# Kernel tuning notes

Measured on AMD Instinct MI355X. Metric: run time of the kernel, lower is better.

## Reference

```python
import jax, jax.numpy as jnp
import numpy as np

E = 100000   # n_entities
R = 64       # n_relations
I = 256      # in_channels
O = 256      # out_channels
N_EDGES = 1_600_000


def setup_inputs() -> dict:
    key = jax.random.key(0)
    k1, k2, k3, k4 = jax.random.split(key, 4)
    x = jax.random.normal(k1, (E, I), dtype=jnp.float32)
    # cs must be nonzero (it is reciprocated); uniform in [0.5, 1.5)
    cs = jax.random.uniform(k2, (E, R), dtype=jnp.float32) + 0.5
    W = jax.random.normal(k3, (R, I, O), dtype=jnp.float32) * 0.05
    edge_index = jax.random.randint(k4, (2, N_EDGES), 0, E, dtype=jnp.int64)
    return {"x": x, "cs": cs, "W": W, "edge_index": edge_index}


def reference(x, cs, W, edge_index):
    # Faithful to: torch.einsum('er,rio,ej->eo', 1/cs, W, x)
    # i and j are independently contracted indices, so this factorizes:
    # out[e,o] = (sum_j x[e,j]) * sum_r (1/cs[e,r]) * (sum_i W[r,i,o])
    cs_reciprocal = 1.0 / cs                 # (E, R)
    W_sum = jnp.sum(W, axis=1)               # (R, O)
    x_sum = jnp.sum(x, axis=1)               # (E,)
    src = (cs_reciprocal @ W_sum) * x_sum[:, None]  # (E, O)
    return src
```

## Files before the change

### kernel.cpp

```cpp
#include <hip/hip_runtime.h>


constexpr int En = 100000;
constexpr int Rn = 64;
constexpr int In = 256;
constexpr int On = 256;

__global__ void wsum_kernel(const float* __restrict__ W, float* __restrict__ wsum) {
    const int r = blockIdx.x >> 3;
    const int chunk = blockIdx.x & 7;
    const int o = threadIdx.x;
    const float* base = W + ((size_t)r * In + (size_t)chunk * 32) * On + o;
    float s = 0.f;
#pragma unroll
    for (int i = 0; i < 32; ++i) s += base[(size_t)i * On];
    atomicAdd(&wsum[r * On + o], s);
}

__global__ __launch_bounds__(256) void rgcn_main(const float* __restrict__ x,
                                                 const float* __restrict__ cs,
                                                 const float* __restrict__ wsum,
                                                 float* __restrict__ out) {
    __shared__ float ldsW[Rn * On];
    __shared__ float recipT[Rn * 64];

    const int t = threadIdx.x;
    const int R0 = blockIdx.x * 64;

#pragma unroll
    for (int k = 0; k < 16; ++k) {
        const int f = k * 1024 + t * 4;
        *reinterpret_cast<float4*>(&ldsW[f]) =
            *reinterpret_cast<const float4*>(&wsum[f]);
    }

    const int wv = t >> 6;
    const int lane = t & 63;
#pragma unroll
    for (int s = 0; s < 16; ++s) {
        const int lr = s * 4 + wv;
        const int g = R0 + lr;
        float4 v = make_float4(0.f, 0.f, 0.f, 0.f);
        if (g < En)
            v = *reinterpret_cast<const float4*>(&x[(size_t)g * In + lane * 4]);
        float sum = v.x + v.y + v.z + v.w;
#pragma unroll
        for (int off = 32; off; off >>= 1) sum += __shfl_down(sum, off, 64);
        if (lane == 0) recipT[lr] = sum;
    }
    __syncthreads();

    const int q = t >> 4;
    const int m = t & 15;
    float xs[4];
    float4 c4[4];
#pragma unroll
    for (int s = 0; s < 4; ++s) {
        const int row = s * 16 + q;
        const int g = R0 + row;
        xs[s] = (g < En) ? recipT[row] : 0.f;
        c4[s] = make_float4(1.f, 1.f, 1.f, 1.f);
        if (g < En)
            c4[s] = *reinterpret_cast<const float4*>(&cs[(size_t)g * Rn + m * 4]);
    }
    __syncthreads();

#pragma unroll
    for (int s = 0; s < 4; ++s) {
        const int row = s * 16 + q;
        recipT[(4 * m + 0) * 64 + row] = xs[s] / c4[s].x;
        recipT[(4 * m + 1) * 64 + row] = xs[s] / c4[s].y;
        recipT[(4 * m + 2) * 64 + row] = xs[s] / c4[s].z;
        recipT[(4 * m + 3) * 64 + row] = xs[s] / c4[s].w;
    }
    __syncthreads();

    const int trow = t >> 5;
    const int tcol = t & 31;
    float acc[8][8];
#pragma unroll
    for (int j = 0; j < 8; ++j)
#pragma unroll
        for (int k = 0; k < 8; ++k) acc[j][k] = 0.f;

#pragma unroll 4
    for (int r = 0; r < 64; ++r) {
        const float4 a0 = *reinterpret_cast<float4*>(&recipT[r * 64 + trow * 8]);
        const float4 a1 = *reinterpret_cast<float4*>(&recipT[r * 64 + trow * 8 + 4]);
        const float4 b0 = *reinterpret_cast<float4*>(&ldsW[r * 256 + tcol * 4]);
        const float4 b1 = *reinterpret_cast<float4*>(&ldsW[r * 256 + 128 + tcol * 4]);
        const float a[8] = {a0.x, a0.y, a0.z, a0.w, a1.x, a1.y, a1.z, a1.w};
        const float b[8] = {b0.x, b0.y, b0.z, b0.w, b1.x, b1.y, b1.z, b1.w};
#pragma unroll
        for (int j = 0; j < 8; ++j)
#pragma unroll
            for (int k = 0; k < 8; ++k)
                acc[j][k] = fmaf(a[j], b[k], acc[j][k]);
    }

#pragma unroll
    for (int j = 0; j < 8; ++j) {
        const int g = R0 + trow * 8 + j;
        if (g < En) {
            const float4 o0 = make_float4(acc[j][0], acc[j][1], acc[j][2], acc[j][3]);
            const float4 o1 = make_float4(acc[j][4], acc[j][5], acc[j][6], acc[j][7]);
            *reinterpret_cast<float4*>(&out[(size_t)g * On + tcol * 4]) = o0;
            *reinterpret_cast<float4*>(&out[(size_t)g * On + 128 + tcol * 4]) = o1;
        }
    }
}

extern "C" void kernel_launch(void* const* d_in, const int* in_sizes, int n_in,
                              void* d_out, int out_size, void* d_ws, size_t ws_size,
                              hipStream_t stream) {
    const float* x  = (const float*)d_in[0];
    const float* cs = (const float*)d_in[1];
    const float* W  = (const float*)d_in[2];
    float* wsum = (float*)d_ws;
    float* out  = (float*)d_out;

    hipMemsetAsync(wsum, 0, Rn * On * sizeof(float), stream);
    wsum_kernel<<<dim3(Rn * 8), dim3(256), 0, stream>>>(W, wsum);
    const int tiles = (En + 63) / 64;
    rgcn_main<<<dim3(tiles), dim3(256), 0, stream>>>(x, cs, wsum, out);
}
```

Measured before the change: 267.7 us.

## Rewrite as bf16 MFMA pipeline with separate x-sum and W-sum kernels

Replaces the fused LDS-tiled FP32 outer-product kernel with three kernels. One reduces W to a transposed bf16 wsum without atomics or memset. One computes row sums of x. The last is a persistent grid-stride kernel that keeps wsum in registers, converts reciprocals of cs to bf16 and uses 16x16x32 bf16 MFMA with software prefetch of the next tile. This removes the FP32 FMA and LDS traffic, but lowers precision to bf16, uses an approximate rcp, and adds an extra kernel launch and an xsum round trip (possibly staged through the output buffer).

```diff
diff --git a/kernel.cpp b/kernel.cpp
--- a/kernel.cpp
+++ b/kernel.cpp
@@ -5,108 +5,129 @@
 constexpr int Rn = 64;
 constexpr int In = 256;
 constexpr int On = 256;
+constexpr int TILES = En / 16;
 
-__global__ void wsum_kernel(const float* __restrict__ W, float* __restrict__ wsum) {
-    const int r = blockIdx.x >> 3;
-    const int chunk = blockIdx.x & 7;
-    const int o = threadIdx.x;
-    const float* base = W + ((size_t)r * In + (size_t)chunk * 32) * On + o;
+typedef short bf16x8 __attribute__((ext_vector_type(8)));
+typedef float floatx4 __attribute__((ext_vector_type(4)));
+
+static __device__ __forceinline__ short f2bf(float f) {
+    unsigned u = __builtin_bit_cast(unsigned, f);
+    unsigned r = (u + 0x7FFFu + ((u >> 16) & 1u)) >> 16;
+    return (short)r;
+}
+
+__global__ __launch_bounds__(1024) void wsum_kernel(const float* __restrict__ W,
+                                                    short* __restrict__ wsumT) {
+    __shared__ float red[16][65];
+    const int r  = blockIdx.x >> 2;
+    const int h  = blockIdx.x & 3;
+    const int ol = threadIdx.x & 63;
+    const int ic = threadIdx.x >> 6;
+    const int o  = h * 64 + ol;
+    const float* base = W + ((size_t)r * In + (size_t)ic * 16) * On + o;
     float s = 0.f;
 #pragma unroll
-    for (int i = 0; i < 32; ++i) s += base[(size_t)i * On];
-    atomicAdd(&wsum[r * On + o], s);
+    for (int i = 0; i < 16; ++i) s += base[(size_t)i * On];
+    red[ic][ol] = s;
+    __syncthreads();
+    if (ic == 0) {
+        float t = 0.f;
+#pragma unroll
+        for (int j = 0; j < 16; ++j) t += red[j][ol];
+        wsumT[o * Rn + r] = f2bf(t);
+    }
 }
 
-__global__ __launch_bounds__(256) void rgcn_main(const float* __restrict__ x,
-                                                 const float* __restrict__ cs,
-                                                 const float* __restrict__ wsum,
-                                                 float* __restrict__ out) {
-    __shared__ float ldsW[Rn * On];
-    __shared__ float recipT[Rn * 64];
+__global__ __launch_bounds__(256) void xsum_kernel(const float* __restrict__ x,
+                                                   float* __restrict__ xsum,
+                                                   int xstride) {
+    const int w    = (blockIdx.x * 256 + (int)threadIdx.x) >> 6;
+    const int nw   = (gridDim.x * 256) >> 6;
+    const int lane = threadIdx.x & 63;
+    for (int base = w * 4; base < En; base += nw * 4) {
+        float s[4];
+#pragma unroll
+        for (int u = 0; u < 4; ++u) {
+            const int row = base + u;
+            float4 v = make_float4(0.f, 0.f, 0.f, 0.f);
+            if (row < En)
+                v = *(const float4*)&x[(size_t)row * In + lane * 4];
+            s[u] = (v.x + v.y) + (v.z + v.w);
+        }
+#pragma unroll
+        for (int u = 0; u < 4; ++u) {
+#pragma unroll
+            for (int off = 32; off; off >>= 1) s[u] += __shfl_down(s[u], off, 64);
+        }
+        if (lane == 0) {
+#pragma unroll
+            for (int u = 0; u < 4; ++u)
+                if (base + u < En) xsum[(size_t)(base + u) * xstride] = s[u];
+        }
+    }
+}
 
-    const int t = threadIdx.x;
-    const int R0 = blockIdx.x * 64;
+__global__ __launch_bounds__(256) void out_kernel(const float* __restrict__ cs,
+                                                  const short* __restrict__ wsumT,
+                                                  const float* __restrict__ xsum,
+                                                  int xstride,
+                                                  float* __restrict__ out) {
+    const int gw = (blockIdx.x * 256 + (int)threadIdx.x) >> 6;
+    const int nw = (gridDim.x * 256) >> 6;
+    const int ln = threadIdx.x & 63;
+    const int lm = ln & 15;
+    const int q  = ln >> 4;
 
+    bf16x8 wa0[16], wa1[16];
 #pragma unroll
-    for (int k = 0; k < 16; ++k) {
-        const int f = k * 1024 + t * 4;
-        *reinterpret_cast<float4*>(&ldsW[f]) =
-            *reinterpret_cast<const float4*>(&wsum[f]);
+    for (int ot = 0; ot < 16; ++ot) {
+        const short* p = wsumT + ((ot * 16 + lm) * Rn + q * 8);
+        wa0[ot] = *(const bf16x8*)p;
+        wa1[ot] = *(const bf16x8*)(p + 32);
     }
 
-    const int wv = t >> 6;
-    const int lane = t & 63;
+    int t = gw;
+    if (t >= TILES) return;
+    float4 c0, c1, c2, c3;
+    float xv;
+    {
+        const float* p = cs + (size_t)(t * 16 + lm) * Rn + q * 8;
+        c0 = *(const float4*)p;        c1 = *(const float4*)(p + 4);
+        c2 = *(const float4*)(p + 32); c3 = *(const float4*)(p + 36);
+        xv = xsum[(size_t)(t * 16 + lm) * xstride];
+    }
+    while (true) {
+        const int tn = t + nw;
+        const float4 d0 = c0, d1 = c1, d2 = c2, d3 = c3;
+        const float xs = xv;
+        if (tn < TILES) {
+            const float* p = cs + (size_t)(tn * 16 + lm) * Rn + q * 8;
+            c0 = *(const float4*)p;        c1 = *(const float4*)(p + 4);
+            c2 = *(const float4*)(p + 32); c3 = *(const float4*)(p + 36);
+            xv = xsum[(size_t)(tn * 16 + lm) * xstride];
+        }
+        bf16x8 b0, b1;
+        {
+            const float rv[16] = {d0.x, d0.y, d0.z, d0.w, d1.x, d1.y, d1.z, d1.w,
+                                  d2.x, d2.y, d2.z, d2.w, d3.x, d3.y, d3.z, d3.w};
 #pragma unroll
-    for (int s = 0; s < 16; ++s) {
-        const int lr = s * 4 + wv;
-        const int g = R0 + lr;
-        float4 v = make_float4(0.f, 0.f, 0.f, 0.f);
-        if (g < En)
-            v = *reinterpret_cast<const float4*>(&x[(size_t)g * In + lane * 4]);
-        float sum = v.x + v.y + v.z + v.w;
+            for (int j = 0; j < 8; ++j) {
+                b0[j] = f2bf(__builtin_amdgcn_rcpf(rv[j]));
+                b1[j] = f2bf(__builtin_amdgcn_rcpf(rv[8 + j]));
+            }
+        }
+        float* orow = out + (size_t)(t * 16 + lm) * On + q * 4;
 #pragma unroll
-        for (int off = 32; off; off >>= 1) sum += __shfl_down(sum, off, 64);
-        if (lane == 0) recipT[lr] = sum;
-    }
-    __syncthreads();
-
-    const int q = t >> 4;
-    const int m = t & 15;
-    float xs[4];
-    float4 c4[4];
-#pragma unroll
-    for (int s = 0; s < 4; ++s) {
-        const int row = s * 16 + q;
-        const int g = R0 + row;
-        xs[s] = (g < En) ? recipT[row] : 0.f;
-        c4[s] = make_float4(1.f, 1.f, 1.f, 1.f);
-        if (g < En)
-            c4[s] = *reinterpret_cast<const float4*>(&cs[(size_t)g * Rn + m * 4]);
-    }
-    __syncthreads();
-
-#pragma unroll
-    for (int s = 0; s < 4; ++s) {
-        const int row = s * 16 + q;
-        recipT[(4 * m + 0) * 64 + row] = xs[s] / c4[s].x;
-        recipT[(4 * m + 1) * 64 + row] = xs[s] / c4[s].y;
-        recipT[(4 * m + 2) * 64 + row] = xs[s] / c4[s].z;
-        recipT[(4 * m + 3) * 64 + row] = xs[s] / c4[s].w;
-    }
-    __syncthreads();
-
-    const int trow = t >> 5;
-    const int tcol = t & 31;
-    float acc[8][8];
-#pragma unroll
-    for (int j = 0; j < 8; ++j)
-#pragma unroll
-        for (int k = 0; k < 8; ++k) acc[j][k] = 0.f;
-
-#pragma unroll 4
-    for (int r = 0; r < 64; ++r) {
-        const float4 a0 = *reinterpret_cast<float4*>(&recipT[r * 64 + trow * 8]);
-        const float4 a1 = *reinterpret_cast<float4*>(&recipT[r * 64 + trow * 8 + 4]);
-        const float4 b0 = *reinterpret_cast<float4*>(&ldsW[r * 256 + tcol * 4]);
-        const float4 b1 = *reinterpret_cast<float4*>(&ldsW[r * 256 + 128 + tcol * 4]);
-        const float a[8] = {a0.x, a0.y, a0.z, a0.w, a1.x, a1.y, a1.z, a1.w};
-        const float b[8] = {b0.x, b0.y, b0.z, b0.w, b1.x, b1.y, b1.z, b1.w};
-#pragma unroll
-        for (int j = 0; j < 8; ++j)
-#pragma unroll
-            for (int k = 0; k < 8; ++k)
-                acc[j][k] = fmaf(a[j], b[k], acc[j][k]);
-    }
-
-#pragma unroll
-    for (int j = 0; j < 8; ++j) {
-        const int g = R0 + trow * 8 + j;
-        if (g < En) {
-            const float4 o0 = make_float4(acc[j][0], acc[j][1], acc[j][2], acc[j][3]);
-            const float4 o1 = make_float4(acc[j][4], acc[j][5], acc[j][6], acc[j][7]);
-            *reinterpret_cast<float4*>(&out[(size_t)g * On + tcol * 4]) = o0;
-            *reinterpret_cast<float4*>(&out[(size_t)g * On + 128 + tcol * 4]) = o1;
+        for (int ot = 0; ot < 16; ++ot) {
+            floatx4 acc = {0.f, 0.f, 0.f, 0.f};
+            acc = __builtin_amdgcn_mfma_f32_16x16x32_bf16(wa0[ot], b0, acc, 0, 0, 0);
+            acc = __builtin_amdgcn_mfma_f32_16x16x32_bf16(wa1[ot], b1, acc, 0, 0, 0);
+            const float4 st = make_float4(acc[0] * xs, acc[1] * xs,
+                                          acc[2] * xs, acc[3] * xs);
+            *(float4*)(orow + ot * 16) = st;
         }
+        if (tn >= TILES) break;
+        t = tn;
     }
 }
 
@@ -116,11 +137,20 @@
     const float* x  = (const float*)d_in[0];
     const float* cs = (const float*)d_in[1];
     const float* W  = (const float*)d_in[2];
-    float* wsum = (float*)d_ws;
-    float* out  = (float*)d_out;
+    float* out = (float*)d_out;
 
-    hipMemsetAsync(wsum, 0, Rn * On * sizeof(float), stream);
-    wsum_kernel<<<dim3(Rn * 8), dim3(256), 0, stream>>>(W, wsum);
-    const int tiles = (En + 63) / 64;
-    rgcn_main<<<dim3(tiles), dim3(256), 0, stream>>>(x, cs, wsum, out);
+    short* wsumT = (short*)d_ws;
+    float* xsum;
+    int xstride;
+    if (ws_size >= (size_t)(32768 + En * 4)) {
+        xsum = (float*)((char*)d_ws + 32768);
+        xstride = 1;
+    } else {
+        xsum = out;
+        xstride = On;
+    }
+
+    wsum_kernel<<<dim3(256), dim3(1024), 0, stream>>>(W, wsumT);
+    xsum_kernel<<<dim3(2048), dim3(256), 0, stream>>>(x, xsum, xstride);
+    out_kernel<<<dim3(512), dim3(256), 0, stream>>>(cs, wsumT, xsum, xstride, out);
 }
```

New measurement: 231.2 us. 1.16x faster.
